# Performance work log

Measured on AMD Instinct MI355X. Metric: run time of the kernel, lower is better.

Reference implementation:

```python
import jax, jax.numpy as jnp
import numpy as np

IN_CAPS, IN_SIZE = 1152, 8
OUT_CAPS, OUT_SIZE = 10, 16
NUM_ITERS = 3


def squash(s, axis=-1, eps=1e-8):
    sq = jnp.sum(s * s, axis=axis, keepdims=True)
    norm = jnp.sqrt(sq + eps)
    return (sq / (1.0 + sq)) * (s / norm)


def setup_inputs() -> dict:
    key = jax.random.key(0)
    kx, kw = jax.random.split(key)
    x = jax.random.normal(kx, (512, IN_CAPS, IN_SIZE), dtype=jnp.float32)
    W = jax.random.normal(kw, (IN_CAPS, OUT_CAPS, OUT_SIZE, IN_SIZE), dtype=jnp.float32)
    return {"x": x, "W": W}


def reference(x, W):
    # u_hat[b,i,o,p] = sum_q W[i,o,p,q] x[b,i,q]   -> [B, I, O, P]
    u_hat = jnp.einsum("iopq,biq->biop", W, x)
    b_ij = jnp.zeros((IN_CAPS, OUT_CAPS), dtype=u_hat.dtype)
    v_j = None
    for _ in range(NUM_ITERS):
        # legacy F.softmax on [1,I,O,1] with no dim -> softmax over dim=1 (in_capsules)
        c_ij = jax.nn.softmax(b_ij, axis=0)                      # [I, O]
        s_j = jnp.einsum("io,biop->bop", c_ij, u_hat)            # [B, O, P]
        v_j = squash(s_j, axis=-1)                               # [B, O, P]
        # agreement, averaged over batch
        u_vj1 = jnp.einsum("biop,bop->io", u_hat, v_j) / x.shape[0]
        b_ij = b_ij + u_vj1
    return v_j  # [B, 10, 16]
```

## Files before the change

### kernel.cpp

```cpp
#include <hip/hip_runtime.h>
#include <hip/hip_bf16.h>

#define B 512
#define IC 1152
#define QD 8
#define OD 10
#define PD 16
#define KD (IC * QD)
#define NKB (KD / 32)
#define NCS 36
#define KSTEPS (NKB / NCS)
#define NCB 4
#define SOP (B * OD * PD)
#define IO (IC * OD)
#define TPX ((B / 64) * (KD / 64))

typedef short bf16x8 __attribute__((ext_vector_type(8)));
typedef short bf16x4 __attribute__((ext_vector_type(4)));
typedef float f32x4 __attribute__((ext_vector_type(4)));

__device__ __forceinline__ short f2bf(float f) {
  union { float f; unsigned u; } x;
  x.f = f;
  unsigned r = x.u + 0x7FFFu + ((x.u >> 16) & 1u);
  return (short)(r >> 16);
}

__global__ __launch_bounds__(256) void prep_kernel(const float* __restrict__ x,
                                                   const float* __restrict__ W,
                                                   float* __restrict__ bijT,
                                                   short* __restrict__ Bs,
                                                   short* __restrict__ xB,
                                                   short* __restrict__ xT) {
  const int bid = blockIdx.x, tid = threadIdx.x;
  if (bid < TPX) {
    __shared__ short lds[64 * 72];
    const int bt = bid / (KD / 64), qt = bid % (KD / 64);
    const int b0 = bt * 64, c0 = qt * 64;
    const int row0 = tid >> 4, col4 = (tid & 15) * 4;
#pragma unroll
    for (int j = 0; j < 4; ++j) {
      const int row = row0 + j * 16;
      const float4 v = *(const float4*)(x + (size_t)(b0 + row) * KD + c0 + col4);
      bf16x4 ov;
      ov[0] = f2bf(v.x); ov[1] = f2bf(v.y); ov[2] = f2bf(v.z); ov[3] = f2bf(v.w);
      *(bf16x4*)(xB + (size_t)(b0 + row) * KD + c0 + col4) = ov;
      lds[(col4 + 0) * 72 + row] = ov[0];
      lds[(col4 + 1) * 72 + row] = ov[1];
      lds[(col4 + 2) * 72 + row] = ov[2];
      lds[(col4 + 3) * 72 + row] = ov[3];
    }
    __syncthreads();
    const int iq = tid & 63, seg = tid >> 6;
    const short* src = lds + iq * 72 + seg * 16;
    short* dst = xT + (size_t)(c0 + iq) * B + b0 + seg * 16;
    *(bf16x8*)dst = *(const bf16x8*)src;
    *(bf16x8*)(dst + 8) = *(const bf16x8*)(src + 8);
    return;
  }
  const int t = (bid - TPX) * 256 + tid;
  if (t < IO) bijT[t] = 0.f;
  const int kb = t / 160, n = t % 160;
  const int o = n >> 4, p = n & 15;
  const float ci = 1.0f / (float)IC;
  short ov[32];
#pragma unroll
  for (int quad = 0; quad < 4; ++quad) {
    const int i = kb * 4 + quad;
    const float4* wp = (const float4*)(W + (((size_t)i * OD + o) * PD + p) * QD);
    const float4 w0 = wp[0], w1 = wp[1];
    ov[quad * 8 + 0] = f2bf(ci * w0.x); ov[quad * 8 + 1] = f2bf(ci * w0.y);
    ov[quad * 8 + 2] = f2bf(ci * w0.z); ov[quad * 8 + 3] = f2bf(ci * w0.w);
    ov[quad * 8 + 4] = f2bf(ci * w1.x); ov[quad * 8 + 5] = f2bf(ci * w1.y);
    ov[quad * 8 + 6] = f2bf(ci * w1.z); ov[quad * 8 + 7] = f2bf(ci * w1.w);
  }
  int4* dst = (int4*)(Bs + (size_t)t * 32);
  const int4* src = (const int4*)ov;
#pragma unroll
  for (int j = 0; j < 4; ++j) dst[j] = src[j];
}

__global__ __launch_bounds__(256) void rbn_kernel(const float* __restrict__ W,
                                                  const float* __restrict__ bijT,
                                                  short* __restrict__ Bs) {
  __shared__ float wred[4][OD];
  __shared__ float invs[OD];
  const int tid = threadIdx.x;
  const int wave = tid >> 6, lane = tid & 63;
  float lsum[OD];
#pragma unroll
  for (int o = 0; o < OD; ++o) lsum[o] = 0.f;
  for (int i = tid; i < IC; i += 256) {
#pragma unroll
    for (int o = 0; o < OD; ++o) lsum[o] += __expf(bijT[(size_t)o * IC + i]);
  }
#pragma unroll
  for (int o = 0; o < OD; ++o) {
    float s = lsum[o];
#pragma unroll
    for (int st = 1; st < 64; st <<= 1) s += __shfl_xor(s, st);
    if (lane == 0) wred[wave][o] = s;
  }
  __syncthreads();
  if (tid < OD)
    invs[tid] = 1.f / (wred[0][tid] + wred[1][tid] + wred[2][tid] + wred[3][tid]);
  __syncthreads();
  const int t = blockIdx.x * 256 + tid;
  const int kb = t / 160, n = t % 160;
  const int o = n >> 4, p = n & 15;
  const float inv = invs[o];
  const float4 bv = *(const float4*)(bijT + (size_t)o * IC + kb * 4);
  float cw[4];
  cw[0] = __expf(bv.x) * inv; cw[1] = __expf(bv.y) * inv;
  cw[2] = __expf(bv.z) * inv; cw[3] = __expf(bv.w) * inv;
  short ov[32];
#pragma unroll
  for (int quad = 0; quad < 4; ++quad) {
    const int i = kb * 4 + quad;
    const float ci = cw[quad];
    const float4* wp = (const float4*)(W + (((size_t)i * OD + o) * PD + p) * QD);
    const float4 w0 = wp[0], w1 = wp[1];
    ov[quad * 8 + 0] = f2bf(ci * w0.x); ov[quad * 8 + 1] = f2bf(ci * w0.y);
    ov[quad * 8 + 2] = f2bf(ci * w0.z); ov[quad * 8 + 3] = f2bf(ci * w0.w);
    ov[quad * 8 + 4] = f2bf(ci * w1.x); ov[quad * 8 + 5] = f2bf(ci * w1.y);
    ov[quad * 8 + 6] = f2bf(ci * w1.z); ov[quad * 8 + 7] = f2bf(ci * w1.w);
  }
  int4* dst = (int4*)(Bs + (size_t)t * 32);
  const int4* src = (const int4*)ov;
#pragma unroll
  for (int j = 0; j < 4; ++j) dst[j] = src[j];
}

__global__ __launch_bounds__(256) void sgemm_kernel(const short* __restrict__ xB,
                                                    const short* __restrict__ Bs,
                                                    float* __restrict__ s_part) {
  const int tid = threadIdx.x;
  const int wave = tid >> 6, lane = tid & 63;
  const int ln = lane & 15, quad = lane >> 4;
  const int cz = blockIdx.x % NCS, mb = blockIdx.x / NCS;
  const int m0 = mb * 64 + wave * 16;
  f32x4 acc[10] = {};
  const short* arow = xB + (size_t)(m0 + ln) * KD + quad * 8;
#pragma unroll
  for (int step = 0; step < KSTEPS; ++step) {
    const int kb = cz * KSTEPS + step;
    const bf16x8 af = *(const bf16x8*)(arow + kb * 32);
    const short* bp = Bs + (size_t)kb * 5120 + ln * 32 + quad * 8;
#pragma unroll
    for (int nt = 0; nt < 10; ++nt) {
      const bf16x8 bf = *(const bf16x8*)(bp + nt * 512);
      acc[nt] = __builtin_amdgcn_mfma_f32_16x16x32_bf16(af, bf, acc[nt], 0, 0, 0);
    }
  }
  float* sp = s_part + (size_t)cz * SOP;
#pragma unroll
  for (int nt = 0; nt < 10; ++nt)
#pragma unroll
    for (int r = 0; r < 4; ++r)
      sp[(size_t)(m0 + quad * 4 + r) * 160 + nt * 16 + ln] = acc[nt][r];
}

__global__ __launch_bounds__(256) void squash_kernel(const float* __restrict__ s_part,
                                                     short* __restrict__ vB,
                                                     float* __restrict__ out,
                                                     int write_out) {
  const int t = blockIdx.x * 256 + threadIdx.x;
  float sv = 0.f;
#pragma unroll 6
  for (int ch = 0; ch < NCS; ++ch) sv += s_part[(size_t)ch * SOP + t];
  float sq = sv * sv;
#pragma unroll
  for (int m = 1; m < 16; m <<= 1) sq += __shfl_xor(sq, m, 16);
  const float norm = sqrtf(sq + 1e-8f);
  const float val = sv * (sq / ((1.f + sq) * norm));
  if (write_out) {
    out[t] = val;
  } else {
    const int b = t / 160, n = t - b * 160;
    vB[((size_t)(b >> 5) * 160 + n) * 32 + (b & 31)] = f2bf(val);
  }
}

__global__ __launch_bounds__(256) void aggemm_kernel(const short* __restrict__ xT,
                                                     const float* __restrict__ W,
                                                     const short* __restrict__ vB,
                                                     float* __restrict__ bijT) {
  const int tid = threadIdx.x;
  const int ig8 = blockIdx.x, kq = blockIdx.y;
  const int mt = tid >> 6, lane = tid & 63;
  const int ln = lane & 15, quad = lane >> 4;
  f32x4 acc[10] = {};
  const short* arow = xT + (size_t)(ig8 * 64 + mt * 16 + ln) * B + kq * 128 + quad * 8;
#pragma unroll
  for (int kb = 0; kb < 4; ++kb) {
    const bf16x8 af = *(const bf16x8*)(arow + kb * 32);
    const short* bp = vB + ((size_t)(kq * 4 + kb) * 160 + ln) * 32 + quad * 8;
#pragma unroll
    for (int nt = 0; nt < 10; ++nt) {
      const bf16x8 bf = *(const bf16x8*)(bp + nt * 512);
      acc[nt] = __builtin_amdgcn_mfma_f32_16x16x32_bf16(af, bf, acc[nt], 0, 0, 0);
    }
  }
  const int i = ig8 * 8 + mt * 2 + (quad >> 1);
  const int qb = (quad & 1) * 4;
#pragma unroll
  for (int nt = 0; nt < 10; ++nt) {
    const float4 wv = *(const float4*)(W + (((size_t)i * OD + nt) * PD + ln) * QD + qb);
    float pa = acc[nt][0] * wv.x + acc[nt][1] * wv.y + acc[nt][2] * wv.z + acc[nt][3] * wv.w;
    pa += __shfl_xor(pa, 1); pa += __shfl_xor(pa, 2); pa += __shfl_xor(pa, 4);
    pa += __shfl_xor(pa, 8); pa += __shfl_xor(pa, 16);
    if ((lane & 31) == 0)
      atomicAdd(&bijT[(size_t)nt * IC + i], pa * (1.0f / (float)B));
  }
}


extern "C" void kernel_launch(void* const* d_in, const int* in_sizes, int n_in,
                              void* d_out, int out_size, void* d_ws, size_t ws_size,
                              hipStream_t stream) {
  const float* x = (const float*)d_in[0];
  const float* W = (const float*)d_in[1];
  float* out = (float*)d_out;

  float* ws = (float*)d_ws;
  float* s_part = ws;
  float* bijT = s_part + (size_t)NCS * SOP;
  short* vB = (short*)(bijT + IO);
  short* Bs = vB + (size_t)16 * 160 * 32;
  short* xB = Bs + (size_t)NKB * 160 * 32;
  short* xT = xB + (size_t)B * KD;

  const dim3 agrid(144, NCB);

  prep_kernel<<<TPX + 180, 256, 0, stream>>>(x, W, bijT, Bs, xB, xT);
  sgemm_kernel<<<8 * NCS, 256, 0, stream>>>(xB, Bs, s_part);
  squash_kernel<<<SOP / 256, 256, 0, stream>>>(s_part, vB, out, 0);
  aggemm_kernel<<<agrid, 256, 0, stream>>>(xT, W, vB, bijT);
  rbn_kernel<<<180, 256, 0, stream>>>(W, bijT, Bs);
  sgemm_kernel<<<8 * NCS, 256, 0, stream>>>(xB, Bs, s_part);
  squash_kernel<<<SOP / 256, 256, 0, stream>>>(s_part, vB, out, 0);
  aggemm_kernel<<<agrid, 256, 0, stream>>>(xT, W, vB, bijT);
  rbn_kernel<<<180, 256, 0, stream>>>(W, bijT, Bs);
  sgemm_kernel<<<8 * NCS, 256, 0, stream>>>(xB, Bs, s_part);
  squash_kernel<<<SOP / 256, 256, 0, stream>>>(s_part, vB, out, 1);
}
```

Measured before the change: 178.1 us.

## Fuse s-GEMM with squash and fold softmax rebuild into agreement kernel

```diff
diff --git a/kernel.cpp b/kernel.cpp
--- a/kernel.cpp
+++ b/kernel.cpp
@@ -8,10 +8,7 @@
 #define PD 16
 #define KD (IC * QD)
 #define NKB (KD / 32)
-#define NCS 36
-#define KSTEPS (NKB / NCS)
 #define NCB 4
-#define SOP (B * OD * PD)
 #define IO (IC * OD)
 #define TPX ((B / 64) * (KD / 64))
 
@@ -29,6 +26,7 @@
 __global__ __launch_bounds__(256) void prep_kernel(const float* __restrict__ x,
                                                    const float* __restrict__ W,
                                                    float* __restrict__ bijT,
+                                                   int* __restrict__ ctr,
                                                    short* __restrict__ Bs,
                                                    short* __restrict__ xB,
                                                    short* __restrict__ xT) {
@@ -60,19 +58,19 @@
   }
   const int t = (bid - TPX) * 256 + tid;
   if (t < IO) bijT[t] = 0.f;
+  if (t < 144) ctr[t] = 0;
   const int kb = t / 160, n = t % 160;
   const int o = n >> 4, p = n & 15;
-  const float ci = 1.0f / (float)IC;
   short ov[32];
 #pragma unroll
   for (int quad = 0; quad < 4; ++quad) {
     const int i = kb * 4 + quad;
     const float4* wp = (const float4*)(W + (((size_t)i * OD + o) * PD + p) * QD);
     const float4 w0 = wp[0], w1 = wp[1];
-    ov[quad * 8 + 0] = f2bf(ci * w0.x); ov[quad * 8 + 1] = f2bf(ci * w0.y);
-    ov[quad * 8 + 2] = f2bf(ci * w0.z); ov[quad * 8 + 3] = f2bf(ci * w0.w);
-    ov[quad * 8 + 4] = f2bf(ci * w1.x); ov[quad * 8 + 5] = f2bf(ci * w1.y);
-    ov[quad * 8 + 6] = f2bf(ci * w1.z); ov[quad * 8 + 7] = f2bf(ci * w1.w);
+    ov[quad * 8 + 0] = f2bf(w0.x); ov[quad * 8 + 1] = f2bf(w0.y);
+    ov[quad * 8 + 2] = f2bf(w0.z); ov[quad * 8 + 3] = f2bf(w0.w);
+    ov[quad * 8 + 4] = f2bf(w1.x); ov[quad * 8 + 5] = f2bf(w1.y);
+    ov[quad * 8 + 6] = f2bf(w1.z); ov[quad * 8 + 7] = f2bf(w1.w);
   }
   int4* dst = (int4*)(Bs + (size_t)t * 32);
   const int4* src = (const int4*)ov;
@@ -80,111 +78,86 @@
   for (int j = 0; j < 4; ++j) dst[j] = src[j];
 }
 
-__global__ __launch_bounds__(256) void rbn_kernel(const float* __restrict__ W,
-                                                  const float* __restrict__ bijT,
-                                                  short* __restrict__ Bs) {
-  __shared__ float wred[4][OD];
-  __shared__ float invs[OD];
-  const int tid = threadIdx.x;
-  const int wave = tid >> 6, lane = tid & 63;
-  float lsum[OD];
-#pragma unroll
-  for (int o = 0; o < OD; ++o) lsum[o] = 0.f;
+__global__ __launch_bounds__(256) void fuse1_kernel(const short* __restrict__ xB,
+                                                    const short* __restrict__ Bs,
+                                                    const float* __restrict__ bijT,
+                                                    short* __restrict__ vB,
+                                                    float* __restrict__ out,
+                                                    int write_out) {
+  __shared__ float sbuf[4][32][33];
+  __shared__ float wr[4][2];
+  const int tid = threadIdx.x, wave = tid >> 6, lane = tid & 63;
+  const int ln = lane & 15, quad = lane >> 4;
+  const int mb = blockIdx.x, o0 = blockIdx.y * 2;
+  float ls0 = 0.f, ls1 = 0.f;
   for (int i = tid; i < IC; i += 256) {
-#pragma unroll
-    for (int o = 0; o < OD; ++o) lsum[o] += __expf(bijT[(size_t)o * IC + i]);
-  }
-#pragma unroll
-  for (int o = 0; o < OD; ++o) {
-    float s = lsum[o];
-#pragma unroll
-    for (int st = 1; st < 64; st <<= 1) s += __shfl_xor(s, st);
-    if (lane == 0) wred[wave][o] = s;
-  }
-  __syncthreads();
-  if (tid < OD)
-    invs[tid] = 1.f / (wred[0][tid] + wred[1][tid] + wred[2][tid] + wred[3][tid]);
-  __syncthreads();
-  const int t = blockIdx.x * 256 + tid;
-  const int kb = t / 160, n = t % 160;
-  const int o = n >> 4, p = n & 15;
-  const float inv = invs[o];
-  const float4 bv = *(const float4*)(bijT + (size_t)o * IC + kb * 4);
-  float cw[4];
-  cw[0] = __expf(bv.x) * inv; cw[1] = __expf(bv.y) * inv;
-  cw[2] = __expf(bv.z) * inv; cw[3] = __expf(bv.w) * inv;
-  short ov[32];
-#pragma unroll
-  for (int quad = 0; quad < 4; ++quad) {
-    const int i = kb * 4 + quad;
-    const float ci = cw[quad];
-    const float4* wp = (const float4*)(W + (((size_t)i * OD + o) * PD + p) * QD);
-    const float4 w0 = wp[0], w1 = wp[1];
-    ov[quad * 8 + 0] = f2bf(ci * w0.x); ov[quad * 8 + 1] = f2bf(ci * w0.y);
-    ov[quad * 8 + 2] = f2bf(ci * w0.z); ov[quad * 8 + 3] = f2bf(ci * w0.w);
-    ov[quad * 8 + 4] = f2bf(ci * w1.x); ov[quad * 8 + 5] = f2bf(ci * w1.y);
-    ov[quad * 8 + 6] = f2bf(ci * w1.z); ov[quad * 8 + 7] = f2bf(ci * w1.w);
-  }
-  int4* dst = (int4*)(Bs + (size_t)t * 32);
-  const int4* src = (const int4*)ov;
-#pragma unroll
-  for (int j = 0; j < 4; ++j) dst[j] = src[j];
-}
-
-__global__ __launch_bounds__(256) void sgemm_kernel(const short* __restrict__ xB,
-                                                    const short* __restrict__ Bs,
-                                                    float* __restrict__ s_part) {
-  const int tid = threadIdx.x;
-  const int wave = tid >> 6, lane = tid & 63;
-  const int ln = lane & 15, quad = lane >> 4;
-  const int cz = blockIdx.x % NCS, mb = blockIdx.x / NCS;
-  const int m0 = mb * 64 + wave * 16;
-  f32x4 acc[10] = {};
-  const short* arow = xB + (size_t)(m0 + ln) * KD + quad * 8;
-#pragma unroll
-  for (int step = 0; step < KSTEPS; ++step) {
-    const int kb = cz * KSTEPS + step;
-    const bf16x8 af = *(const bf16x8*)(arow + kb * 32);
-    const short* bp = Bs + (size_t)kb * 5120 + ln * 32 + quad * 8;
-#pragma unroll
-    for (int nt = 0; nt < 10; ++nt) {
-      const bf16x8 bf = *(const bf16x8*)(bp + nt * 512);
-      acc[nt] = __builtin_amdgcn_mfma_f32_16x16x32_bf16(af, bf, acc[nt], 0, 0, 0);
-    }
-  }
-  float* sp = s_part + (size_t)cz * SOP;
-#pragma unroll
-  for (int nt = 0; nt < 10; ++nt)
-#pragma unroll
-    for (int r = 0; r < 4; ++r)
-      sp[(size_t)(m0 + quad * 4 + r) * 160 + nt * 16 + ln] = acc[nt][r];
-}
-
-__global__ __launch_bounds__(256) void squash_kernel(const float* __restrict__ s_part,
-                                                     short* __restrict__ vB,
-                                                     float* __restrict__ out,
-                                                     int write_out) {
-  const int t = blockIdx.x * 256 + threadIdx.x;
-  float sv = 0.f;
-#pragma unroll 6
-  for (int ch = 0; ch < NCS; ++ch) sv += s_part[(size_t)ch * SOP + t];
-  float sq = sv * sv;
-#pragma unroll
-  for (int m = 1; m < 16; m <<= 1) sq += __shfl_xor(sq, m, 16);
-  const float norm = sqrtf(sq + 1e-8f);
-  const float val = sv * (sq / ((1.f + sq) * norm));
-  if (write_out) {
-    out[t] = val;
-  } else {
-    const int b = t / 160, n = t - b * 160;
-    vB[((size_t)(b >> 5) * 160 + n) * 32 + (b & 31)] = f2bf(val);
-  }
-}
-
-__global__ __launch_bounds__(256) void aggemm_kernel(const short* __restrict__ xT,
-                                                     const float* __restrict__ W,
-                                                     const short* __restrict__ vB,
-                                                     float* __restrict__ bijT) {
+    ls0 += __expf(bijT[(size_t)o0 * IC + i]);
+    ls1 += __expf(bijT[(size_t)(o0 + 1) * IC + i]);
+  }
+#pragma unroll
+  for (int st = 1; st < 64; st <<= 1) {
+    ls0 += __shfl_xor(ls0, st);
+    ls1 += __shfl_xor(ls1, st);
+  }
+  if (lane == 0) { wr[wave][0] = ls0; wr[wave][1] = ls1; }
+  const int m0 = mb * 32;
+  f32x4 acc00 = {}, acc01 = {}, acc10 = {}, acc11 = {};
+  const short* arow0 = xB + (size_t)(m0 + ln) * KD + quad * 8;
+  const short* arow1 = arow0 + (size_t)16 * KD;
+  const short* bbase = Bs + (size_t)wave * 72 * 5120 + o0 * 512 + ln * 32 + quad * 8;
+#pragma unroll 8
+  for (int step = 0; step < 72; ++step) {
+    const int kb = wave * 72 + step;
+    const bf16x8 a0 = *(const bf16x8*)(arow0 + (size_t)kb * 32);
+    const bf16x8 a1 = *(const bf16x8*)(arow1 + (size_t)kb * 32);
+    const short* bp = bbase + (size_t)step * 5120;
+    const bf16x8 b0 = *(const bf16x8*)bp;
+    const bf16x8 b1 = *(const bf16x8*)(bp + 512);
+    acc00 = __builtin_amdgcn_mfma_f32_16x16x32_bf16(a0, b0, acc00, 0, 0, 0);
+    acc10 = __builtin_amdgcn_mfma_f32_16x16x32_bf16(a1, b0, acc10, 0, 0, 0);
+    acc01 = __builtin_amdgcn_mfma_f32_16x16x32_bf16(a0, b1, acc01, 0, 0, 0);
+    acc11 = __builtin_amdgcn_mfma_f32_16x16x32_bf16(a1, b1, acc11, 0, 0, 0);
+  }
+#pragma unroll
+  for (int r = 0; r < 4; ++r) {
+    sbuf[wave][quad * 4 + r][ln] = acc00[r];
+    sbuf[wave][quad * 4 + r][16 + ln] = acc01[r];
+    sbuf[wave][16 + quad * 4 + r][ln] = acc10[r];
+    sbuf[wave][16 + quad * 4 + r][16 + ln] = acc11[r];
+  }
+  __syncthreads();
+  const float inv0 = 1.f / (wr[0][0] + wr[1][0] + wr[2][0] + wr[3][0]);
+  const float inv1 = 1.f / (wr[0][1] + wr[1][1] + wr[2][1] + wr[3][1]);
+  const int p = tid & 15, r0 = tid >> 4;
+#pragma unroll
+  for (int rr = 0; rr < 2; ++rr) {
+    const int row = r0 + rr * 16;
+#pragma unroll
+    for (int ol = 0; ol < 2; ++ol) {
+      const int col = ol * 16 + p;
+      float sv = (sbuf[0][row][col] + sbuf[1][row][col] + sbuf[2][row][col] +
+                  sbuf[3][row][col]) * (ol ? inv1 : inv0);
+      float sq = sv * sv;
+#pragma unroll
+      for (int m = 1; m < 16; m <<= 1) sq += __shfl_xor(sq, m, 16);
+      const float norm = sqrtf(sq + 1e-8f);
+      const float val = sv * (sq / ((1.f + sq) * norm));
+      const int b = m0 + row, n = (o0 + ol) * 16 + p;
+      if (write_out) {
+        out[(size_t)b * 160 + n] = val;
+      } else {
+        vB[((size_t)(b >> 5) * 160 + n) * 32 + (b & 31)] = f2bf(val);
+      }
+    }
+  }
+}
+
+__global__ __launch_bounds__(256) void agg2_kernel(const short* __restrict__ xT,
+                                                   const float* __restrict__ W,
+                                                   const short* __restrict__ vB,
+                                                   float* __restrict__ bijT,
+                                                   short* __restrict__ Bs,
+                                                   int* __restrict__ ctr) {
   const int tid = threadIdx.x;
   const int ig8 = blockIdx.x, kq = blockIdx.y;
   const int mt = tid >> 6, lane = tid & 63;
@@ -203,6 +176,7 @@
   }
   const int i = ig8 * 8 + mt * 2 + (quad >> 1);
   const int qb = (quad & 1) * 4;
+  float rsum = 0.f;
 #pragma unroll
   for (int nt = 0; nt < 10; ++nt) {
     const float4 wv = *(const float4*)(W + (((size_t)i * OD + nt) * PD + ln) * QD + qb);
@@ -210,7 +184,46 @@
     pa += __shfl_xor(pa, 1); pa += __shfl_xor(pa, 2); pa += __shfl_xor(pa, 4);
     pa += __shfl_xor(pa, 8); pa += __shfl_xor(pa, 16);
     if ((lane & 31) == 0)
-      atomicAdd(&bijT[(size_t)nt * IC + i], pa * (1.0f / (float)B));
+      rsum += atomicAdd(&bijT[(size_t)nt * IC + i], pa * (1.0f / (float)B));
+  }
+  asm volatile("" :: "v"(rsum));
+  __syncthreads();
+  __shared__ int flag;
+  __shared__ float eL[8][OD];
+  if (tid == 0)
+    flag = (__hip_atomic_fetch_add(&ctr[ig8], 1, __ATOMIC_RELAXED,
+                                   __HIP_MEMORY_SCOPE_AGENT) == NCB - 1) ? 1 : 0;
+  __syncthreads();
+  if (!flag) return;
+  if (tid < 8 * OD) {
+    const int il = tid / OD, o = tid - il * OD;
+    const float bv = __hip_atomic_load(&bijT[(size_t)o * IC + ig8 * 8 + il],
+                                       __ATOMIC_RELAXED, __HIP_MEMORY_SCOPE_AGENT);
+    eL[il][o] = __expf(bv);
+  }
+  if (tid == 0)
+    __hip_atomic_store(&ctr[ig8], 0, __ATOMIC_RELAXED, __HIP_MEMORY_SCOPE_AGENT);
+  __syncthreads();
+  for (int vb = tid; vb < 320; vb += 256) {
+    const int kbl = vb / 160, n = vb - kbl * 160;
+    const int kb = ig8 * 2 + kbl;
+    const int o = n >> 4, pp = n & 15;
+    short ov[32];
+#pragma unroll
+    for (int q4 = 0; q4 < 4; ++q4) {
+      const int ii = kb * 4 + q4;
+      const float ci = eL[ii - ig8 * 8][o];
+      const float4* wp = (const float4*)(W + (((size_t)ii * OD + o) * PD + pp) * QD);
+      const float4 w0 = wp[0], w1 = wp[1];
+      ov[q4 * 8 + 0] = f2bf(ci * w0.x); ov[q4 * 8 + 1] = f2bf(ci * w0.y);
+      ov[q4 * 8 + 2] = f2bf(ci * w0.z); ov[q4 * 8 + 3] = f2bf(ci * w0.w);
+      ov[q4 * 8 + 4] = f2bf(ci * w1.x); ov[q4 * 8 + 5] = f2bf(ci * w1.y);
+      ov[q4 * 8 + 6] = f2bf(ci * w1.z); ov[q4 * 8 + 7] = f2bf(ci * w1.w);
+    }
+    int4* dst = (int4*)(Bs + (size_t)(kb * 160 + n) * 32);
+    const int4* src = (const int4*)ov;
+#pragma unroll
+    for (int j = 0; j < 4; ++j) dst[j] = src[j];
   }
 }
 
@@ -222,25 +235,20 @@
   const float* W = (const float*)d_in[1];
   float* out = (float*)d_out;
 
-  float* ws = (float*)d_ws;
-  float* s_part = ws;
-  float* bijT = s_part + (size_t)NCS * SOP;
-  short* vB = (short*)(bijT + IO);
+  float* bijT = (float*)d_ws;
+  int* ctr = (int*)(bijT + IO);
+  short* vB = (short*)(ctr + 160);
   short* Bs = vB + (size_t)16 * 160 * 32;
   short* xB = Bs + (size_t)NKB * 160 * 32;
   short* xT = xB + (size_t)B * KD;
 
+  const dim3 fgrid(16, 5);
   const dim3 agrid(144, NCB);
 
-  prep_kernel<<<TPX + 180, 256, 0, stream>>>(x, W, bijT, Bs, xB, xT);
-  sgemm_kernel<<<8 * NCS, 256, 0, stream>>>(xB, Bs, s_part);
-  squash_kernel<<<SOP / 256, 256, 0, stream>>>(s_part, vB, out, 0);
-  aggemm_kernel<<<agrid, 256, 0, stream>>>(xT, W, vB, bijT);
-  rbn_kernel<<<180, 256, 0, stream>>>(W, bijT, Bs);
-  sgemm_kernel<<<8 * NCS, 256, 0, stream>>>(xB, Bs, s_part);
-  squash_kernel<<<SOP / 256, 256, 0, stream>>>(s_part, vB, out, 0);
-  aggemm_kernel<<<agrid, 256, 0, stream>>>(xT, W, vB, bijT);
-  rbn_kernel<<<180, 256, 0, stream>>>(W, bijT, Bs);
-  sgemm_kernel<<<8 * NCS, 256, 0, stream>>>(xB, Bs, s_part);
-  squash_kernel<<<SOP / 256, 256, 0, stream>>>(s_part, vB, out, 1);
-}
+  prep_kernel<<<TPX + 180, 256, 0, stream>>>(x, W, bijT, ctr, Bs, xB, xT);
+  fuse1_kernel<<<fgrid, 256, 0, stream>>>(xB, Bs, bijT, vB, out, 0);
+  agg2_kernel<<<agrid, 256, 0, stream>>>(xT, W, vB, bijT, Bs, ctr);
+  fuse1_kernel<<<fgrid, 256, 0, stream>>>(xB, Bs, bijT, vB, out, 0);
+  agg2_kernel<<<agrid, 256, 0, stream>>>(xT, W, vB, bijT, Bs, ctr);
+  fuse1_kernel<<<fgrid, 256, 0, stream>>>(xB, Bs, bijT, vB, out, 1);
+}
```

Result: slower. 208.6 us (+17.1%).
